# Kernel optimization log

Hardware: AMD Instinct MI355X
Metric: run time of the kernel (lower is better)

The kernel has to match this reference:

```python
import jax, jax.numpy as jnp
import numpy as np

B = 4096        # batch
T = 365         # encoder sequence length
H = 64          # hidden size
HORIZON = 7


def setup_inputs() -> dict:
    key = jax.random.key(0)
    ks = jax.random.split(key, 16)
    s = 0.05
    w = lambda k, shape: (jax.random.normal(k, shape, dtype=jnp.float32) * s)
    return {
        "x": jax.random.normal(ks[0], (B, T, 1), dtype=jnp.float32),
        "enc_Wih0": w(ks[1], (4 * H, 1)),
        "enc_Whh0": w(ks[2], (4 * H, H)),
        "enc_b0": w(ks[3], (4 * H,)),
        "enc_Wih1": w(ks[4], (4 * H, H)),
        "enc_Whh1": w(ks[5], (4 * H, H)),
        "enc_b1": w(ks[6], (4 * H,)),
        "dec_Wih0": w(ks[7], (4 * H, 1)),
        "dec_Whh0": w(ks[8], (4 * H, H)),
        "dec_b0": w(ks[9], (4 * H,)),
        "dec_Wih1": w(ks[10], (4 * H, H)),
        "dec_Whh1": w(ks[11], (4 * H, H)),
        "dec_b1": w(ks[12], (4 * H,)),
        "fc_W": w(ks[13], (1, H)),
        "fc_b": w(ks[14], (1,)),
    }


def _lstm_cell(xt, h, c, Wih, Whh, b):
    # PyTorch gate order: input, forget, cell(g), output
    gates = xt @ Wih.T + h @ Whh.T + b  # [B, 4H]
    i, f, g, o = jnp.split(gates, 4, axis=-1)
    c_new = jax.nn.sigmoid(f) * c + jax.nn.sigmoid(i) * jnp.tanh(g)
    h_new = jax.nn.sigmoid(o) * jnp.tanh(c_new)
    return h_new, c_new


def _run_layer(seq, Wih, Whh, b):
    # seq: [T, B, in] -> hidden seq [T, B, H], final (h, c)
    bsz = seq.shape[1]
    h0 = jnp.zeros((bsz, H), seq.dtype)
    c0 = jnp.zeros((bsz, H), seq.dtype)

    def step(carry, xt):
        h, c = carry
        h, c = _lstm_cell(xt, h, c, Wih, Whh, b)
        return (h, c), h

    (hF, cF), hs = jax.lax.scan(step, (h0, c0), seq)
    return hs, hF, cF


def reference(x, enc_Wih0, enc_Whh0, enc_b0, enc_Wih1, enc_Whh1, enc_b1,
              dec_Wih0, dec_Whh0, dec_b0, dec_Wih1, dec_Whh1, dec_b1,
              fc_W, fc_b):
    xT = jnp.transpose(x, (1, 0, 2))  # [T, B, 1]
    hs0, h0, c0 = _run_layer(xT, enc_Wih0, enc_Whh0, enc_b0)
    _, h1, c1 = _run_layer(hs0, enc_Wih1, enc_Whh1, enc_b1)

    dec_in = jnp.zeros((x.shape[0], 1), x.dtype)  # [B, 1]
    outs = []
    for _ in range(HORIZON):
        h0, c0 = _lstm_cell(dec_in, h0, c0, dec_Wih0, dec_Whh0, dec_b0)
        h1, c1 = _lstm_cell(h0, h1, c1, dec_Wih1, dec_Whh1, dec_b1)
        pred = h1 @ fc_W.T + fc_b  # [B, 1]
        outs.append(pred)
        dec_in = pred
    return jnp.stack(outs, axis=1)  # [B, HORIZON, 1]
```

## Files before the change

### kernel.cpp

```cpp
#include <hip/hip_runtime.h>


typedef _Float16 f16x8 __attribute__((ext_vector_type(8)));
typedef _Float16 f16x4 __attribute__((ext_vector_type(4)));
typedef float    f32x4 __attribute__((ext_vector_type(4)));
typedef float    f32x2 __attribute__((ext_vector_type(2)));

static constexpr int T_ENC = 365;
static constexpr int HZ    = 7;
static constexpr int BT    = 16;
static constexpr int HPAD  = 72;

static constexpr float LOG2E  = 1.442695040888963f;
static constexpr float SCL_I  = -LOG2E;
static constexpr float SCL_G  = 2.0f * LOG2E;

#if __has_builtin(__builtin_amdgcn_exp2f)
__device__ __forceinline__ float fexp2(float x) { return __builtin_amdgcn_exp2f(x); }
#else
__device__ __forceinline__ float fexp2(float x) { return __exp2f(x); }
#endif
#if __has_builtin(__builtin_amdgcn_rcpf)
__device__ __forceinline__ float frcp(float x) { return __builtin_amdgcn_rcpf(x); }
#else
__device__ __forceinline__ float frcp(float x) { return 1.0f / x; }
#endif

__device__ __forceinline__ f32x4 mm1(f16x8 w, f16x8 a, f32x4 acc) {
  return __builtin_amdgcn_mfma_f32_16x16x32_f16(w, a, acc, 0, 0, 0);
}

__global__ __launch_bounds__(512, 2)
void lstm_fused(const float* __restrict__ x,
                const float* __restrict__ eWih0, const float* __restrict__ eWhh0,
                const float* __restrict__ eb0,
                const float* __restrict__ eWih1, const float* __restrict__ eWhh1,
                const float* __restrict__ eb1,
                const float* __restrict__ dWih0, const float* __restrict__ dWhh0,
                const float* __restrict__ db0,
                const float* __restrict__ dWih1, const float* __restrict__ dWhh1,
                const float* __restrict__ db1,
                const float* __restrict__ fcW, const float* __restrict__ fcb,
                float* __restrict__ out)
{
  __shared__ __align__(16) float    xs[(T_ENC + 1) * BT];
  __shared__ __align__(16) _Float16 h0s[2][BT * HPAD];
  __shared__ __align__(16) _Float16 h1s[2][BT * HPAD];
  __shared__ __align__(16) float    pdec[BT * 4];

  const int tid  = threadIdx.x;
  const int lane = tid & 63;
  const int wv   = tid >> 6;
  const int wg   = wv & 3;
  const int n    = lane & 15;
  const int q    = lane >> 4;
  const int b0g  = blockIdx.x * BT;
  const int nH   = n * HPAD;
  const int cbase = (wg << 4) + (q << 2);

#if __has_builtin(__builtin_amdgcn_s_setprio)
  if (wv >= 4) __builtin_amdgcn_s_setprio(1);
#endif

  for (int i = tid; i < T_ENC * BT; i += 512) {
    int b = i / T_ENC;
    int t = i - b * T_ENC;
    xs[t * BT + b] = x[(b0g + b) * T_ENC + t];
  }
  for (int i = tid; i < 2 * BT * HPAD; i += 512) {
    ((_Float16*)h0s)[i] = (_Float16)0.f;
    ((_Float16*)h1s)[i] = (_Float16)0.f;
  }

  f16x8 WA[4][2], WB[4][2];
  f32x4 biasq[4], wih0q[4];

  auto gscale = [&](int ti) { return (ti == 2) ? SCL_G : SCL_I; };

  auto cvtrow = [&](const float* p, float s, f16x8& w) {
    #pragma unroll
    for (int j = 0; j < 8; ++j) w[j] = (_Float16)(p[j] * s);
  };
  auto loadA = [&](const float* Wih0_, const float* Whh0_, const float* b0_) {
    #pragma unroll
    for (int ti = 0; ti < 4; ++ti) {
      const float s = gscale(ti);
      const int rw = (ti * 4 + wg) * 16 + n;
      const int rq = (ti * 4 + wg) * 16 + (q << 2);
      #pragma unroll
      for (int rr = 0; rr < 4; ++rr) {
        biasq[ti][rr] = b0_[rq + rr] * s;
        wih0q[ti][rr] = Wih0_[rq + rr] * s;
      }
      #pragma unroll
      for (int kc = 0; kc < 2; ++kc)
        cvtrow(Whh0_ + rw * 64 + kc * 32 + q * 8, s, WA[ti][kc]);
    }
  };
  auto loadB = [&](const float* Wih1_, const float* Whh1_, const float* b1_) {
    #pragma unroll
    for (int ti = 0; ti < 4; ++ti) {
      const float s = gscale(ti);
      const int rw = (ti * 4 + wg) * 16 + n;
      const int rq = (ti * 4 + wg) * 16 + (q << 2);
      #pragma unroll
      for (int rr = 0; rr < 4; ++rr) biasq[ti][rr] = b1_[rq + rr] * s;
      #pragma unroll
      for (int kc = 0; kc < 2; ++kc) {
        cvtrow(Wih1_ + rw * 64 + kc * 32 + q * 8, s, WA[ti][kc]);
        cvtrow(Whh1_ + rw * 64 + kc * 32 + q * 8, s, WB[ti][kc]);
      }
    }
  };

  if (wv < 4) loadA(eWih0, eWhh0, eb0);
  else        loadB(eWih1, eWhh1, eb1);

  f32x2 cp[2] = {{0.f, 0.f}, {0.f, 0.f}};

  auto act2 = [&](f32x2 a0, f32x2 a1, f32x2 a2, f32x2 a3, f32x2& c) -> f32x2 {
    f32x2 eg, ef, ei, eo;
    eg.x = fexp2(a2.x); eg.y = fexp2(a2.y);
    ef.x = fexp2(a1.x); ef.y = fexp2(a1.y);
    ei.x = fexp2(a0.x); ei.y = fexp2(a0.y);
    eo.x = fexp2(a3.x); eo.y = fexp2(a3.y);
    const f32x2 one = {1.f, 1.f};
    f32x2 dg = one + eg, df = one + ef, di = one + ei, dd = one + eo;
    f32x2 nd  = eg * df - df;
    f32x2 dif = di * df;
    f32x2 dic = di * c;
    f32x2 t1  = dif * dg;
    f32x2 pc  = dic * dg;
    f32x2 s   = pc + nd;
    const f32x2 sclg = {SCL_G, SCL_G};
    f32x2 sg  = sclg * s;
    f32x2 R1; R1.x = frcp(t1.x); R1.y = frcp(t1.y);
    c = R1 * s;
    f32x2 ca = R1 * sg;
    f32x2 ec; ec.x = fexp2(ca.x); ec.y = fexp2(ca.y);
    f32x2 t2 = ec * dd + dd;
    f32x2 nc = ec - one;
    f32x2 R2; R2.x = frcp(t2.x); R2.y = frcp(t2.y);
    return nc * R2;
  };

  auto epilogue = [&](const f32x4* g, _Float16* O) -> f16x4 {
    f32x2 h2[2];
    #pragma unroll
    for (int pr = 0; pr < 2; ++pr) {
      f32x2 a0 = {g[0][2 * pr], g[0][2 * pr + 1]};
      f32x2 a1 = {g[1][2 * pr], g[1][2 * pr + 1]};
      f32x2 a2 = {g[2][2 * pr], g[2][2 * pr + 1]};
      f32x2 a3 = {g[3][2 * pr], g[3][2 * pr + 1]};
      h2[pr] = act2(a0, a1, a2, a3, cp[pr]);
    }
    f16x4 hv;
    hv[0] = (_Float16)h2[0].x; hv[1] = (_Float16)h2[0].y;
    hv[2] = (_Float16)h2[1].x; hv[3] = (_Float16)h2[1].y;
    *(f16x4*)(O + nH + cbase) = hv;
    return hv;
  };

  auto stepA = [&](const _Float16* H, _Float16* O, float xb) {
    const _Float16* hp = H + nH;
    f16x8 a0 = *(const f16x8*)(hp + q * 8);
    f16x8 a1 = *(const f16x8*)(hp + 32 + q * 8);
    const f32x4 xbv = {xb, xb, xb, xb};
    f32x4 g[4];
    #pragma unroll
    for (int k = 0; k < 4; ++k) {
      constexpr int TO[4] = {2, 1, 0, 3};
      const int ti = TO[k];
      f32x4 ci = biasq[ti] + xbv * wih0q[ti];
      f32x4 a = mm1(WA[ti][0], a0, ci);
      a = mm1(WA[ti][1], a1, a);
      g[ti] = a;
    }
    epilogue(g, O);
  };

  auto stepB = [&](const _Float16* H0, const _Float16* H1, _Float16* O) -> f16x4 {
    const _Float16* p0 = H0 + nH;
    const _Float16* p1 = H1 + nH;
    f16x8 b0 = *(const f16x8*)(p0 + q * 8);
    f16x8 b1 = *(const f16x8*)(p0 + 32 + q * 8);
    f16x8 a0 = *(const f16x8*)(p1 + q * 8);
    f16x8 a1 = *(const f16x8*)(p1 + 32 + q * 8);
    f32x4 g[4];
    #pragma unroll
    for (int k = 0; k < 4; ++k) {
      constexpr int TO[4] = {2, 1, 0, 3};
      const int ti = TO[k];
      f32x4 a = mm1(WA[ti][0], b0, biasq[ti]);
      a = mm1(WA[ti][1], b1, a);
      a = mm1(WB[ti][0], a0, a);
      a = mm1(WB[ti][1], a1, a);
      g[ti] = a;
    }
    return epilogue(g, O);
  };

  __syncthreads();


  float xb_next;
  if (wv < 4) {
    float xb = xs[n];
    stepA(h0s[1], h0s[0], xb);
    xb_next = xs[BT + n];
  }
  __syncthreads();

  for (int s = 1; s <= 363; s += 2) {
    if (wv < 4) {
      stepA(h0s[0], h0s[1], xb_next);
      xb_next = xs[(s + 1) * BT + n];
    } else {
      stepB(h0s[0], h1s[1], h1s[0]);
    }
    __syncthreads();
    if (wv < 4) {
      stepA(h0s[1], h0s[0], xb_next);
      xb_next = xs[(s + 2) * BT + n];
    } else {
      stepB(h0s[1], h1s[0], h1s[1]);
    }
    __syncthreads();
  }

  if (wv < 4) loadA(dWih0, dWhh0, db0);
  else        stepB(h0s[0], h1s[1], h1s[0]);
  __syncthreads();

  if (wv >= 4) loadB(dWih1, dWhh1, db1);
  float fcwq[4];
  #pragma unroll
  for (int j = 0; j < 4; ++j) fcwq[j] = fcW[cbase + j];
  const float fcb0 = fcb[0];

  #pragma unroll 1
  for (int hz = 0; hz < HZ; ++hz) {
    const int p = hz & 1;
    if (wv < 4) {
      float dv = 0.f;
      if (hz > 0) {
        f32x4 pd = *(const f32x4*)&pdec[n << 2];
        dv = ((pd[0] + pd[1]) + (pd[2] + pd[3])) + fcb0;
        if (wv == 0 && lane < BT) out[(b0g + lane) * HZ + (hz - 1)] = dv;
      }
      stepA(h0s[p], h0s[1 - p], dv);
    }
    __syncthreads();
    if (wv >= 4) {
      f16x4 hv = stepB(h0s[1 - p], h1s[p], h1s[1 - p]);
      float pl = fcwq[0] * (float)hv[0];
      pl += fcwq[1] * (float)hv[1];
      pl += fcwq[2] * (float)hv[2];
      pl += fcwq[3] * (float)hv[3];
      pl += __shfl_xor(pl, 16);
      pl += __shfl_xor(pl, 32);
      if (q == 0) pdec[(n << 2) + wg] = pl;
    }
    __syncthreads();
  }
  if (wv == 0 && lane < BT) {
    f32x4 pd = *(const f32x4*)&pdec[lane << 2];
    out[(b0g + lane) * HZ + (HZ - 1)] =
        ((pd[0] + pd[1]) + (pd[2] + pd[3])) + fcb0;
  }
}

extern "C" void kernel_launch(void* const* d_in, const int* in_sizes, int n_in,
                              void* d_out, int out_size, void* d_ws, size_t ws_size,
                              hipStream_t stream) {
  (void)in_sizes; (void)n_in; (void)d_ws; (void)ws_size; (void)out_size;
  const float* x     = (const float*)d_in[0];
  const float* eWih0 = (const float*)d_in[1];
  const float* eWhh0 = (const float*)d_in[2];
  const float* eb0   = (const float*)d_in[3];
  const float* eWih1 = (const float*)d_in[4];
  const float* eWhh1 = (const float*)d_in[5];
  const float* eb1   = (const float*)d_in[6];
  const float* dWih0 = (const float*)d_in[7];
  const float* dWhh0 = (const float*)d_in[8];
  const float* db0   = (const float*)d_in[9];
  const float* dWih1 = (const float*)d_in[10];
  const float* dWhh1 = (const float*)d_in[11];
  const float* db1   = (const float*)d_in[12];
  const float* fcW   = (const float*)d_in[13];
  const float* fcb   = (const float*)d_in[14];
  float* out = (float*)d_out;

  dim3 grid(4096 / BT);
  dim3 block(512);
  hipLaunchKernelGGL(lstm_fused, grid, block, 0, stream,
                     x, eWih0, eWhh0, eb0, eWih1, eWhh1, eb1,
                     dWih0, dWhh0, db0, dWih1, dWhh1, db1, fcW, fcb, out);
}
```

Measured before the change: 315.8 us.

## Split LSTM gate activations across twice as many waves per block

Doubles the block to 1024 threads, so each 16-column gate tile is handled by two waves. Both waves compute the full MFMA gate tile, and each applies the nonlinearities to only two of the four rows. This is meant to shorten the serial per-timestep activation latency on the recurrent critical path. The costs are duplicated MFMA work, heavier barriers with 16 waves, tighter register limits, and a wider partial-sum buffer for the decoder projection.

Result: slower. 566.7 us (+79.5%).

```diff
diff --git a/kernel.cpp b/kernel.cpp
--- a/kernel.cpp
+++ b/kernel.cpp
@@ -2,7 +2,7 @@
 
 
 typedef _Float16 f16x8 __attribute__((ext_vector_type(8)));
-typedef _Float16 f16x4 __attribute__((ext_vector_type(4)));
+typedef _Float16 f16x2 __attribute__((ext_vector_type(2)));
 typedef float    f32x4 __attribute__((ext_vector_type(4)));
 typedef float    f32x2 __attribute__((ext_vector_type(2)));
 
@@ -30,7 +30,7 @@
   return __builtin_amdgcn_mfma_f32_16x16x32_f16(w, a, acc, 0, 0, 0);
 }
 
-__global__ __launch_bounds__(512, 2)
+__global__ __launch_bounds__(1024, 4)
 void lstm_fused(const float* __restrict__ x,
                 const float* __restrict__ eWih0, const float* __restrict__ eWhh0,
                 const float* __restrict__ eb0,
@@ -46,28 +46,31 @@
   __shared__ __align__(16) float    xs[(T_ENC + 1) * BT];
   __shared__ __align__(16) _Float16 h0s[2][BT * HPAD];
   __shared__ __align__(16) _Float16 h1s[2][BT * HPAD];
-  __shared__ __align__(16) float    pdec[BT * 4];
+  __shared__ __align__(16) float    pdec[BT * 8];
 
   const int tid  = threadIdx.x;
   const int lane = tid & 63;
   const int wv   = tid >> 6;
-  const int wg   = wv & 3;
+  const bool isA = (wv < 8);
+  const int sub  = isA ? wv : (wv - 8);
+  const int ub   = sub >> 1;
+  const int prow = sub & 1;
   const int n    = lane & 15;
   const int q    = lane >> 4;
   const int b0g  = blockIdx.x * BT;
   const int nH   = n * HPAD;
-  const int cbase = (wg << 4) + (q << 2);
+  const int cbase = (ub << 4) + (q << 2);
 
 #if __has_builtin(__builtin_amdgcn_s_setprio)
-  if (wv >= 4) __builtin_amdgcn_s_setprio(1);
+  if (!isA) __builtin_amdgcn_s_setprio(1);
 #endif
 
-  for (int i = tid; i < T_ENC * BT; i += 512) {
+  for (int i = tid; i < T_ENC * BT; i += 1024) {
     int b = i / T_ENC;
     int t = i - b * T_ENC;
     xs[t * BT + b] = x[(b0g + b) * T_ENC + t];
   }
-  for (int i = tid; i < 2 * BT * HPAD; i += 512) {
+  for (int i = tid; i < 2 * BT * HPAD; i += 1024) {
     ((_Float16*)h0s)[i] = (_Float16)0.f;
     ((_Float16*)h1s)[i] = (_Float16)0.f;
   }
@@ -85,8 +88,8 @@
     #pragma unroll
     for (int ti = 0; ti < 4; ++ti) {
       const float s = gscale(ti);
-      const int rw = (ti * 4 + wg) * 16 + n;
-      const int rq = (ti * 4 + wg) * 16 + (q << 2);
+      const int rw = (ti * 4 + ub) * 16 + n;
+      const int rq = (ti * 4 + ub) * 16 + (q << 2);
       #pragma unroll
       for (int rr = 0; rr < 4; ++rr) {
         biasq[ti][rr] = b0_[rq + rr] * s;
@@ -101,8 +104,8 @@
     #pragma unroll
     for (int ti = 0; ti < 4; ++ti) {
       const float s = gscale(ti);
-      const int rw = (ti * 4 + wg) * 16 + n;
-      const int rq = (ti * 4 + wg) * 16 + (q << 2);
+      const int rw = (ti * 4 + ub) * 16 + n;
+      const int rq = (ti * 4 + ub) * 16 + (q << 2);
       #pragma unroll
       for (int rr = 0; rr < 4; ++rr) biasq[ti][rr] = b1_[rq + rr] * s;
       #pragma unroll
@@ -113,10 +116,10 @@
     }
   };
 
-  if (wv < 4) loadA(eWih0, eWhh0, eb0);
-  else        loadB(eWih1, eWhh1, eb1);
-
-  f32x2 cp[2] = {{0.f, 0.f}, {0.f, 0.f}};
+  if (isA) loadA(eWih0, eWhh0, eb0);
+  else     loadB(eWih1, eWhh1, eb1);
+
+  f32x2 cp = {0.f, 0.f};
 
   auto act2 = [&](f32x2 a0, f32x2 a1, f32x2 a2, f32x2 a3, f32x2& c) -> f32x2 {
     f32x2 eg, ef, ei, eo;
@@ -144,20 +147,15 @@
     return nc * R2;
   };
 
-  auto epilogue = [&](const f32x4* g, _Float16* O) -> f16x4 {
-    f32x2 h2[2];
-    #pragma unroll
-    for (int pr = 0; pr < 2; ++pr) {
-      f32x2 a0 = {g[0][2 * pr], g[0][2 * pr + 1]};
-      f32x2 a1 = {g[1][2 * pr], g[1][2 * pr + 1]};
-      f32x2 a2 = {g[2][2 * pr], g[2][2 * pr + 1]};
-      f32x2 a3 = {g[3][2 * pr], g[3][2 * pr + 1]};
-      h2[pr] = act2(a0, a1, a2, a3, cp[pr]);
-    }
-    f16x4 hv;
-    hv[0] = (_Float16)h2[0].x; hv[1] = (_Float16)h2[0].y;
-    hv[2] = (_Float16)h2[1].x; hv[3] = (_Float16)h2[1].y;
-    *(f16x4*)(O + nH + cbase) = hv;
+  auto epilogue = [&](const f32x4* g, _Float16* O) -> f16x2 {
+    f32x2 a0 = {g[0][2 * prow], g[0][2 * prow + 1]};
+    f32x2 a1 = {g[1][2 * prow], g[1][2 * prow + 1]};
+    f32x2 a2 = {g[2][2 * prow], g[2][2 * prow + 1]};
+    f32x2 a3 = {g[3][2 * prow], g[3][2 * prow + 1]};
+    f32x2 h2 = act2(a0, a1, a2, a3, cp);
+    f16x2 hv;
+    hv[0] = (_Float16)h2.x; hv[1] = (_Float16)h2.y;
+    *(f16x2*)(O + nH + cbase + 2 * prow) = hv;
     return hv;
   };
 
@@ -179,7 +177,7 @@
     epilogue(g, O);
   };
 
-  auto stepB = [&](const _Float16* H0, const _Float16* H1, _Float16* O) -> f16x4 {
+  auto stepB = [&](const _Float16* H0, const _Float16* H1, _Float16* O) -> f16x2 {
     const _Float16* p0 = H0 + nH;
     const _Float16* p1 = H1 + nH;
     f16x8 b0 = *(const f16x8*)(p0 + q * 8);
@@ -204,7 +202,7 @@
 
 
   float xb_next;
-  if (wv < 4) {
+  if (isA) {
     float xb = xs[n];
     stepA(h0s[1], h0s[0], xb);
     xb_next = xs[BT + n];
@@ -212,14 +210,14 @@
   __syncthreads();
 
   for (int s = 1; s <= 363; s += 2) {
-    if (wv < 4) {
+    if (isA) {
       stepA(h0s[0], h0s[1], xb_next);
       xb_next = xs[(s + 1) * BT + n];
     } else {
       stepB(h0s[0], h1s[1], h1s[0]);
     }
     __syncthreads();
-    if (wv < 4) {
+    if (isA) {
       stepA(h0s[1], h0s[0], xb_next);
       xb_next = xs[(s + 2) * BT + n];
     } else {
@@ -228,45 +226,47 @@
     __syncthreads();
   }
 
-  if (wv < 4) loadA(dWih0, dWhh0, db0);
-  else        stepB(h0s[0], h1s[1], h1s[0]);
+  if (isA) loadA(dWih0, dWhh0, db0);
+  else     stepB(h0s[0], h1s[1], h1s[0]);
   __syncthreads();
 
-  if (wv >= 4) loadB(dWih1, dWhh1, db1);
-  float fcwq[4];
+  if (!isA) loadB(dWih1, dWhh1, db1);
+  float fcwq[2];
   #pragma unroll
-  for (int j = 0; j < 4; ++j) fcwq[j] = fcW[cbase + j];
+  for (int j = 0; j < 2; ++j) fcwq[j] = fcW[cbase + 2 * prow + j];
   const float fcb0 = fcb[0];
 
   #pragma unroll 1
   for (int hz = 0; hz < HZ; ++hz) {
     const int p = hz & 1;
-    if (wv < 4) {
+    if (isA) {
       float dv = 0.f;
       if (hz > 0) {
-        f32x4 pd = *(const f32x4*)&pdec[n << 2];
-        dv = ((pd[0] + pd[1]) + (pd[2] + pd[3])) + fcb0;
+        f32x4 pa = *(const f32x4*)&pdec[n << 3];
+        f32x4 pb = *(const f32x4*)&pdec[(n << 3) + 4];
+        f32x4 ps = pa + pb;
+        dv = ((ps[0] + ps[1]) + (ps[2] + ps[3])) + fcb0;
         if (wv == 0 && lane < BT) out[(b0g + lane) * HZ + (hz - 1)] = dv;
       }
       stepA(h0s[p], h0s[1 - p], dv);
     }
     __syncthreads();
-    if (wv >= 4) {
-      f16x4 hv = stepB(h0s[1 - p], h1s[p], h1s[1 - p]);
+    if (!isA) {
+      f16x2 hv = stepB(h0s[1 - p], h1s[p], h1s[1 - p]);
       float pl = fcwq[0] * (float)hv[0];
       pl += fcwq[1] * (float)hv[1];
-      pl += fcwq[2] * (float)hv[2];
-      pl += fcwq[3] * (float)hv[3];
       pl += __shfl_xor(pl, 16);
       pl += __shfl_xor(pl, 32);
-      if (q == 0) pdec[(n << 2) + wg] = pl;
+      if (q == 0) pdec[(n << 3) + sub] = pl;
     }
     __syncthreads();
   }
   if (wv == 0 && lane < BT) {
-    f32x4 pd = *(const f32x4*)&pdec[lane << 2];
+    f32x4 pa = *(const f32x4*)&pdec[lane << 3];
+    f32x4 pb = *(const f32x4*)&pdec[(lane << 3) + 4];
+    f32x4 ps = pa + pb;
     out[(b0g + lane) * HZ + (HZ - 1)] =
-        ((pd[0] + pd[1]) + (pd[2] + pd[3])) + fcb0;
+        ((ps[0] + ps[1]) + (ps[2] + ps[3])) + fcb0;
   }
 }
 
@@ -292,7 +292,7 @@
   float* out = (float*)d_out;
 
   dim3 grid(4096 / BT);
-  dim3 block(512);
+  dim3 block(1024);
   hipLaunchKernelGGL(lstm_fused, grid, block, 0, stream,
                      x, eWih0, eWhh0, eb0, eWih1, eWhh1, eb1,
                      dWih0, dWhh0, db0, dWih1, dWhh1, db1, fcW, fcb, out);
```
